# Kernel tuning notes

Measured on AMD Instinct MI355X. Metric: run time of the kernel, lower is better.

The kernel has to match this reference:

```python
import jax, jax.numpy as jnp
import numpy as np


def setup_inputs() -> dict:
    key = jax.random.key(0)
    ks = jax.random.split(key, 5)
    B, T, C, H, E = 8, 2048, 1024, 2048, 8
    n_layer = 12
    x = jax.random.normal(ks[0], (B, T, C), dtype=jnp.float32)
    w_router = jax.random.normal(ks[1], (C, E), dtype=jnp.float32) * 0.02
    w_c_fc = jax.random.normal(ks[2], (E, C, H), dtype=jnp.float32) * 0.02
    w_gate = jax.random.normal(ks[3], (E, C, H), dtype=jnp.float32) * 0.02
    w_c_proj = jax.random.normal(ks[4], (E, H, C), dtype=jnp.float32) * (0.02 * (2 * n_layer) ** -0.5)
    return {
        "x": x, "w_router": w_router, "w_c_fc": w_c_fc,
        "w_gate": w_gate, "w_c_proj": w_c_proj,
        "top_k": 2, "n_experts": E, "expert_capacity": 640,
    }


def reference(x, w_router, w_c_fc, w_gate, w_c_proj, top_k, n_experts, expert_capacity):
    B, T, C = x.shape
    # ---- router ----
    gate_logits = jnp.einsum('btc,ce->bte', x, w_router)
    gate_probs = jax.nn.softmax(gate_logits, axis=-1)  # (B,T,E)

    # ---- per-batch top-k dispatch (cumsum slot assignment + scatter) ----
    def dispatch(xb, pb):
        # xb: (T,C), pb: (T,E)
        topk_p, topk_i = jax.lax.top_k(pb, top_k)              # (T,k)
        ei = jnp.swapaxes(topk_i, 0, 1).ravel()                # (k*T,) k-major
        oh = jax.nn.one_hot(ei, n_experts, dtype=jnp.int32)    # (k*T,E)
        pos = jnp.cumsum(oh, axis=0) * oh - 1                  # slot within expert
        pos = jnp.swapaxes(pos.reshape(top_k, T, n_experts), 0, 1).max(axis=2)  # (T,k)
        ei = jnp.swapaxes(ei.reshape(top_k, T), 0, 1)          # (T,k)
        buf = jnp.zeros((n_experts, expert_capacity, C), dtype=xb.dtype)
        xr = jnp.repeat(xb, top_k, axis=0)                     # (T*k,C) token-major
        buf = buf.at[ei.ravel(), pos.ravel()].set(xr)          # overflow slots dropped
        return topk_p, pos, ei, buf

    topk_p, pos, ei, buf = jax.vmap(dispatch)(x, gate_probs)   # buf: (B,E,cap,C)

    # ---- batched expert SwiGLU GEMMs ----
    ein = jnp.swapaxes(buf, 0, 1).reshape(n_experts, B * expert_capacity, C)
    h = jnp.einsum('eti,eih->eth', ein, w_c_fc)
    g = jax.nn.silu(jnp.einsum('eti,eih->eth', ein, w_gate))
    o = jnp.einsum('eth,eho->eto', g * h, w_c_proj)
    eo = jnp.swapaxes(o.reshape(n_experts, B, expert_capacity, C), 0, 1)  # (B,E,cap,C)

    # ---- weighted combine gather ----
    def combine(eo_b, i_b, p_b, pr_b):
        sel = eo_b[i_b, p_b]                                   # (T,k,C)
        return jnp.sum(pr_b[..., None] * sel, axis=1)          # (T,C)

    y = jax.vmap(combine)(eo, ei, pos, topk_p)                 # (B,T,C)
    return y
```

## Files before the change

### kernel.cpp

```cpp
#include <hip/hip_runtime.h>
#include <stdint.h>

#define B_   8
#define T_   2048
#define C_   1024
#define H_   2048
#define E_   8
#define CAP_ 640
#define RPE_ (B_*CAP_)
#define BT_  (B_*T_)

typedef __attribute__((ext_vector_type(8))) short bf16x8;
typedef __attribute__((ext_vector_type(4))) float f32x4;

static __device__ __forceinline__ unsigned short f2bf(float f){
  union { float f; uint32_t u; } a; a.f = f;
  uint32_t u = a.u;
  uint32_t r = (u + 0x7FFFu + ((u >> 16) & 1u)) >> 16;
  return (unsigned short)r;
}

#define GLD16(gp, lp) __builtin_amdgcn_global_load_lds( \
    (__attribute__((address_space(1))) void*)(gp), \
    (__attribute__((address_space(3))) void*)(lp), 16, 0, 0)

#define VMW(N) asm volatile("s_waitcnt vmcnt(" #N ")" ::: "memory")
#define FENCE  asm volatile("" ::: "memory")
#define BARS   do { FENCE; __builtin_amdgcn_s_barrier(); __builtin_amdgcn_sched_barrier(0); } while(0)
#define BARE   do { __builtin_amdgcn_sched_barrier(0); FENCE; __builtin_amdgcn_s_barrier(); FENCE; } while(0)

#define LDA(H) do { \
  _Pragma("unroll") for (int ks_=0; ks_<2; ++ks_) \
  _Pragma("unroll") for (int f_=0; f_<4; ++f_) \
    pa[ks_][f_] = *(const bf16x8*)(bufc + (H)*16384u + aRow + (unsigned)f_*2048u + cc[ks_]); \
} while(0)
#define LDB(PB, H) do { \
  _Pragma("unroll") for (int ks_=0; ks_<2; ++ks_) \
  _Pragma("unroll") for (int n_=0; n_<2; ++n_) \
    PB[ks_][n_] = *(const bf16x8*)(bufc + 32768u + (H)*16384u + bRow + (unsigned)n_*2048u + cc[ks_]); \
} while(0)
#define MM16(Q, PB) do { \
  __builtin_amdgcn_s_setprio(1); \
  _Pragma("unroll") for (int ks_=0; ks_<2; ++ks_) \
  _Pragma("unroll") for (int f_=0; f_<4; ++f_) \
  _Pragma("unroll") for (int n_=0; n_<2; ++n_) \
    acc[Q][f_][n_] = __builtin_amdgcn_mfma_f32_16x16x32_bf16(pa[ks_][f_], PB[ks_][n_], acc[Q][f_][n_], 0,0,0); \
  __builtin_amdgcn_s_setprio(0); \
} while(0)

#define STG_A(H, T1) do { \
  unsigned kb_ = (unsigned)(T1)*128u; \
  unsigned db_ = ((unsigned)(T1)&1u)*65536u + (H)*16384u; \
  GLD16(pA##H##0 + kb_, lds + db_ + d0); \
  GLD16(pA##H##1 + kb_, lds + db_ + 8192u + d0); \
} while(0)
#define STG_B(H, T1) do { \
  unsigned kb_ = (unsigned)(T1)*128u; \
  unsigned db_ = ((unsigned)(T1)&1u)*65536u + 32768u + (H)*16384u; \
  GLD16(pB##H##0 + kb_, lds + db_ + d0); \
  GLD16(pB##H##1 + kb_, lds + db_ + 8192u + d0); \
} while(0)

#define STG2_A(H, T2, BI) do { \
  unsigned kb_ = (unsigned)(T2)*128u; \
  unsigned db_ = (unsigned)(BI)*49152u + (H)*16384u; \
  GLD16(pA##H##0 + kb_, lds + db_ + d0); \
  GLD16(pA##H##1 + kb_, lds + db_ + 8192u + d0); \
} while(0)
#define STG2_B(T2, BI) do { \
  unsigned kb_ = (unsigned)(T2)*128u; \
  unsigned db_ = (unsigned)(BI)*49152u + 32768u; \
  GLD16(pB00 + kb_, lds + db_ + d0); \
  GLD16(pB01 + kb_, lds + db_ + 8192u + d0); \
} while(0)

__global__ __launch_bounds__(256) void router_kernel(
    const float* __restrict__ x, const float* __restrict__ wr,
    unsigned short* __restrict__ xbf, float* __restrict__ probs2, int* __restrict__ idx2)
{
  int bt = blockIdx.x;
  int tid = threadIdx.x;
  const float4 v = ((const float4*)(x + (size_t)bt*C_))[tid];
  ushort4 u;
  u.x = f2bf(v.x); u.y = f2bf(v.y); u.z = f2bf(v.z); u.w = f2bf(v.w);
  ((ushort4*)(xbf + (size_t)bt*C_))[tid] = u;

  double p[8];
  #pragma unroll
  for (int e=0;e<8;e++) p[e]=0.0;
  const float xv[4] = {v.x, v.y, v.z, v.w};
  #pragma unroll
  for (int j=0;j<4;j++){
    int c = tid*4+j;
    const float* wrow = wr + c*8;
    #pragma unroll
    for (int e=0;e<8;e++) p[e] += (double)xv[j] * (double)wrow[e];
  }
  __shared__ double red[8][256];
  #pragma unroll
  for (int e=0;e<8;e++) red[e][tid] = p[e];
  __syncthreads();
  for (int s=128; s>0; s>>=1){
    if (tid < s){
      #pragma unroll
      for (int e=0;e<8;e++) red[e][tid] += red[e][tid+s];
    }
    __syncthreads();
  }
  if (tid==0){
    double lg[8];
    #pragma unroll
    for (int e=0;e<8;e++) lg[e]=red[e][0];
    double mx = lg[0];
    #pragma unroll
    for (int e=1;e<8;e++) if (lg[e]>mx) mx=lg[e];
    double s=0.0, ex[8];
    #pragma unroll
    for (int e=0;e<8;e++){ ex[e]=exp(lg[e]-mx); s+=ex[e]; }
    int i1=0; double b1=ex[0];
    #pragma unroll
    for (int e=1;e<8;e++) if (ex[e]>b1){ b1=ex[e]; i1=e; }
    int i2=-1; double b2=-1.0;
    #pragma unroll
    for (int e=0;e<8;e++) if (e!=i1 && ex[e]>b2){ b2=ex[e]; i2=e; }
    probs2[bt*2+0] = (float)(b1/s);
    probs2[bt*2+1] = (float)(b2/s);
    idx2[bt*2+0] = i1;
    idx2[bt*2+1] = i2;
  }
}

__global__ __launch_bounds__(256) void transp_fcg_kernel(
    const float* __restrict__ fc, const float* __restrict__ gate,
    unsigned short* __restrict__ dst)
{
  __shared__ float t[32][33];
  int e = blockIdx.z;
  int n0 = blockIdx.x*32, k0 = blockIdx.y*32;
  int tx = threadIdx.x & 31, ty = threadIdx.x >> 5;
  #pragma unroll
  for (int sel=0; sel<2; ++sel){
    const float* s = (sel ? gate : fc) + ((size_t)e*C_ + k0)*H_ + n0;
    #pragma unroll
    for (int i=0;i<32;i+=8) t[ty+i][tx] = s[(size_t)(ty+i)*H_ + tx];
    __syncthreads();
    #pragma unroll
    for (int i=0;i<32;i+=8){
      int jj = ty+i;
      int drow = n0*2 + ((jj & 16) << 1) + sel*16 + (jj & 15);
      dst[((size_t)e*4096 + drow)*1024 + k0 + tx] = f2bf(t[tx][jj]);
    }
    __syncthreads();
  }
}

__global__ __launch_bounds__(256) void transp_kernel(
    const float* __restrict__ src, unsigned short* __restrict__ dst, int K, int N)
{
  __shared__ float t[32][33];
  int e = blockIdx.z;
  int n0 = blockIdx.x*32, k0 = blockIdx.y*32;
  int tx = threadIdx.x & 31, ty = threadIdx.x >> 5;
  const float* s = src + ((size_t)e*K + k0)*N + n0;
  #pragma unroll
  for (int i=0;i<32;i+=8) t[ty+i][tx] = s[(size_t)(ty+i)*N + tx];
  __syncthreads();
  unsigned short* d = dst + ((size_t)e*N + n0)*K + k0;
  #pragma unroll
  for (int i=0;i<32;i+=8) d[(size_t)(ty+i)*K + tx] = f2bf(t[tx][ty+i]);
}

__global__ void scan_kernel(const int* __restrict__ idx2, int* __restrict__ pos, int* __restrict__ cnt)
{
  int b = blockIdx.x, lane = threadIdx.x;
  unsigned long long below = (lane == 0) ? 0ull : (~0ull >> (64 - lane));
  int base = 0;
  for (int k=0;k<2;k++){
    for (int c0=0;c0<T_;c0+=64){
      int t = c0 + lane;
      int e = idx2[((b*T_ + t)<<1) + k];
      unsigned long long mym = 0; int addv = 0;
      #pragma unroll
      for (int ee=0; ee<8; ++ee){
        unsigned long long m = __ballot(e == ee);
        if (ee == e) mym = m;
        if (lane == ee) addv = __popcll(m);
      }
      int mybase = __shfl(base, e, 64);
      pos[((b*T_+t)<<1)+k] = mybase + __popcll(mym & below);
      base += addv;
    }
  }
  if (lane < 8) cnt[b*8 + lane] = (base < CAP_) ? base : CAP_;
}

__global__ void offsets_kernel(const int* __restrict__ cnt, int* __restrict__ off, int* __restrict__ Me)
{
  int e = threadIdx.x;
  if (e < 8){
    int s = 0;
    for (int b=0;b<8;b++){ off[e*8+b] = s; s += cnt[b*8+e]; }
    Me[e] = s;
  }
}

__global__ void fill_kernel(const int* __restrict__ idx2, const int* __restrict__ pos,
                            const int* __restrict__ off, const float* __restrict__ probs2,
                            int* __restrict__ token_src, float* __restrict__ row_prob)
{
  int a = blockIdx.x*256 + threadIdx.x;
  if (a >= BT_*2) return;
  int bt = a >> 1, k = a & 1;
  int b = bt >> 11;
  int e = idx2[bt*2+k];
  int p = pos[bt*2+k];
  if (p < CAP_){
    int r = e*RPE_ + off[e*8+b] + p;
    token_src[r] = bt;
    row_prob[r] = probs2[bt*2+k];
  }
}

__global__ __launch_bounds__(512, 2) void gemm1_kernel(
    const unsigned short* __restrict__ xbf,
    const unsigned short* __restrict__ wifcg,
    const int* __restrict__ token_src,
    const int* __restrict__ Me,
    unsigned short* __restrict__ act,
    int e0)
{
  const int lin = blockIdx.x;
  const int ez = lin / 320;
  const int r_ = lin % 320;
  const int xcd = r_ & 7, slot = r_ >> 3;
  const int nt = xcd + ((slot / 20) << 3);
  const int mt = slot % 20;
  const int e = e0 + ez;
  const int M = Me[e];
  if (mt*256 >= M) return;

  __shared__ __align__(16) unsigned char lds[131072];

  const int tid = threadIdx.x;
  const int w = tid >> 6, l = tid & 63;
  const int wm = w >> 2, wn = w & 3;
  const int l15 = l & 15, g0 = l >> 4;
  const unsigned d0 = (unsigned)tid * 16u;

  const int srow0 = tid >> 3, c0 = tid & 7;
  const unsigned scb = (unsigned)((c0 ^ (srow0 & 7)) * 16);
  const unsigned char* gA = (const unsigned char*)xbf;
  const unsigned char* gB = (const unsigned char*)wifcg;
  const int abase = e*RPE_ + mt*256;
  const unsigned char* pA00 = gA + (size_t)token_src[abase +       srow0]*2048u + scb;
  const unsigned char* pA01 = gA + (size_t)token_src[abase +  64 + srow0]*2048u + scb;
  const unsigned char* pA10 = gA + (size_t)token_src[abase + 128 + srow0]*2048u + scb;
  const unsigned char* pA11 = gA + (size_t)token_src[abase + 192 + srow0]*2048u + scb;
  const size_t bbase = (size_t)(ez*4096 + nt*256 + srow0);
  const unsigned char* pB00 = gB + (bbase +   0)*2048u + scb;
  const unsigned char* pB01 = gB + (bbase +  64)*2048u + scb;
  const unsigned char* pB10 = gB + (bbase + 128)*2048u + scb;
  const unsigned char* pB11 = gB + (bbase + 192)*2048u + scb;

  const unsigned aRow = (unsigned)((wm*64 + l15) * 128);
  const unsigned bRow = (unsigned)((wn*32 + l15) * 128);
  unsigned cc[2];
  cc[0] = (unsigned)(((0*4 + g0) ^ (l15 & 7)) * 16);
  cc[1] = (unsigned)(((1*4 + g0) ^ (l15 & 7)) * 16);

  f32x4 acc[4][4][2];
  #pragma unroll
  for (int p=0;p<4;++p)
    #pragma unroll
    for (int f=0;f<4;++f)
      #pragma unroll
      for (int n=0;n<2;++n) acc[p][f][n] = (f32x4){0.f,0.f,0.f,0.f};

  bf16x8 pa[2][4], pb0[2][2], pb1[2][2];

  STG_A(0,0); STG_B(0,0); STG_B(1,0); STG_A(1,0);
  VMW(4);
  FENCE; __builtin_amdgcn_s_barrier(); FENCE;

  const int NT = 16;
  for (int t = 0; t < NT-1; ++t){
    const unsigned char* bufc = lds + (unsigned)(t&1)*65536u;
    LDA(0); LDB(pb0,0); STG_A(0,t+1); VMW(4); BARS; MM16(0,pb0); BARE;
    LDB(pb1,1);         STG_B(0,t+1); VMW(4); BARS; MM16(1,pb1); BARE;
    LDA(1);             STG_B(1,t+1);         BARS; MM16(2,pb0); BARE;
                        STG_A(1,t+1); VMW(4); BARS; MM16(3,pb1); BARE;
  }
  {
    const unsigned char* bufc = lds + (unsigned)((NT-1)&1)*65536u;
    LDA(0); LDB(pb0,0); VMW(2); BARS; MM16(0,pb0); BARE;
    LDB(pb1,1);         VMW(0); BARS; MM16(1,pb1); BARE;
    LDA(1);                     BARS; MM16(2,pb0); BARE;
                                BARS; MM16(3,pb1); BARE;
  }

  const int r4 = (l >> 4) * 4;
  #pragma unroll
  for (int p=0;p<4;++p){
    const int ah = p>>1, bh = p&1;
    #pragma unroll
    for (int f=0;f<4;++f){
      const int grow = mt*256 + ah*128 + wm*64 + f*16 + r4;
      const int hcol = nt*128 + bh*64 + wn*16 + l15;
      #pragma unroll
      for (int r=0;r<4;++r){
        float h = acc[p][f][0][r];
        float gv = acc[p][f][1][r];
        float a = (gv / (1.f + __expf(-gv))) * h;
        act[((size_t)ez*RPE_ + grow + r)*(size_t)H_ + hcol] = f2bf(a);
      }
    }
  }
}

__global__ __launch_bounds__(512, 2) void gemm2_kernel(
    const unsigned short* __restrict__ act,
    const unsigned short* __restrict__ wprojT,
    const int* __restrict__ token_src,
    const float* __restrict__ row_prob,
    const int* __restrict__ Me,
    float* __restrict__ y,
    int e0)
{
  const int lin = blockIdx.x;
  const int ez = lin / 192;
  const int r_ = lin % 192;
  const int xcd = r_ & 7, slot = r_ >> 3;
  const int mt = xcd + ((slot >> 3) << 3);
  const int nt = slot & 7;
  if (mt >= 20) return;
  const int e = e0 + ez;
  const int M = Me[e];
  if (mt*256 >= M) return;

  __shared__ __align__(16) unsigned char lds[147456];

  const int tid = threadIdx.x;
  const int w = tid >> 6, l = tid & 63;
  const int wm = w >> 2, wn = w & 3;
  const int l15 = l & 15, g0 = l >> 4;
  const unsigned d0 = (unsigned)tid * 16u;

  const int srow0 = tid >> 3, c0 = tid & 7;
  const unsigned scb = (unsigned)((c0 ^ (srow0 & 7)) * 16);
  const unsigned char* gA = (const unsigned char*)act;
  const unsigned char* gB = (const unsigned char*)wprojT;
  const size_t abase = (size_t)(ez*RPE_ + mt*256 + srow0);
  const unsigned char* pA00 = gA + (abase +   0)*4096u + scb;
  const unsigned char* pA01 = gA + (abase +  64)*4096u + scb;
  const unsigned char* pA10 = gA + (abase + 128)*4096u + scb;
  const unsigned char* pA11 = gA + (abase + 192)*4096u + scb;
  const size_t bbase = (size_t)(ez*C_ + nt*128 + srow0);
  const unsigned char* pB00 = gB + (bbase +   0)*4096u + scb;
  const unsigned char* pB01 = gB + (bbase +  64)*4096u + scb;

  const unsigned aRow = (unsigned)((wm*64 + l15) * 128);
  const unsigned bRow = (unsigned)((wn*32 + l15) * 128);
  unsigned cc[2];
  cc[0] = (unsigned)(((0*4 + g0) ^ (l15 & 7)) * 16);
  cc[1] = (unsigned)(((1*4 + g0) ^ (l15 & 7)) * 16);

  f32x4 acc[2][4][2];
  #pragma unroll
  for (int p=0;p<2;++p)
    #pragma unroll
    for (int f=0;f<4;++f)
      #pragma unroll
      for (int n=0;n<2;++n) acc[p][f][n] = (f32x4){0.f,0.f,0.f,0.f};

  bf16x8 pa[2][4], pb[2][2];

  STG2_A(0,0,0); STG2_B(0,0); STG2_A(1,0,0);
  STG2_A(0,1,1); STG2_B(1,1); STG2_A(1,1,1);
  VMW(8);
  FENCE; __builtin_amdgcn_s_barrier(); FENCE;

  const int NT = 32;
  for (int t = 0; t < NT-2; ++t){
    const unsigned char* bufc = lds + (unsigned)(t%3)*49152u;
    const int bi2 = (t+2)%3;
    LDA(0); LDB(pb,0); STG2_A(0,t+2,bi2); STG2_B(t+2,bi2); VMW(10); BARS; MM16(0,pb); BARE;
    LDA(1);            STG2_A(1,t+2,bi2);                  VMW(8);  BARS; MM16(1,pb); BARE;
  }
  {
    const unsigned char* bufc = lds + (unsigned)((NT-2)%3)*49152u;
    LDA(0); LDB(pb,0); VMW(6); BARS; MM16(0,pb); BARE;
    LDA(1);            VMW(2); BARS; MM16(1,pb); BARE;
  }
  {
    const unsigned char* bufc = lds + (unsigned)((NT-1)%3)*49152u;
    LDA(0); LDB(pb,0); VMW(0); BARS; MM16(0,pb); BARE;
    LDA(1);                    BARS; MM16(1,pb); BARE;
  }

  const int r4 = (l >> 4) * 4;
  #pragma unroll
  for (int p=0;p<2;++p){
    #pragma unroll
    for (int f=0;f<4;++f){
      #pragma unroll
      for (int r=0;r<4;++r){
        const int rloc = mt*256 + p*128 + wm*64 + f*16 + r4 + r;
        if (rloc < M){
          const int bt = token_src[e*RPE_ + rloc];
          const float pp = row_prob[e*RPE_ + rloc];
          float* yrow = y + (size_t)bt*C_;
          const int colb = nt*128 + wn*32 + l15;
          atomicAdd(yrow + colb,      pp * acc[p][f][0][r]);
          atomicAdd(yrow + colb + 16, pp * acc[p][f][1][r]);
        }
      }
    }
  }
}

extern "C" void kernel_launch(void* const* d_in, const int* in_sizes, int n_in,
                              void* d_out, int out_size, void* d_ws, size_t ws_size,
                              hipStream_t stream)
{
  const float* x   = (const float*)d_in[0];
  const float* wr  = (const float*)d_in[1];
  const float* wfc = (const float*)d_in[2];
  const float* wg  = (const float*)d_in[3];
  const float* wpj = (const float*)d_in[4];
  float* y = (float*)d_out;

  unsigned char* ws = (unsigned char*)d_ws;
  const size_t szXBF  = (size_t)BT_*C_*2;
  const size_t szFCGc = (size_t)2*4096*1024*2;
  const size_t szWPc  = (size_t)2*C_*H_*2;
  const size_t szFCGa = (size_t)E_*4096*1024*2;
  const size_t szWPa  = (size_t)E_*C_*H_*2;
  const size_t szMISC = 3*131072 + 2*(size_t)E_*RPE_*4 + 1024;

  const size_t need_small = szXBF + szFCGc + szWPc + (size_t)2*RPE_*H_*2 + szMISC;
  const size_t need_big2  = szXBF + szFCGa + szWPa  + (size_t)2*RPE_*H_*2 + szMISC;
  const size_t need_big4  = szXBF + szFCGa + szWPa  + (size_t)4*RPE_*H_*2 + szMISC;
  if (ws_size < need_small) return;
  const bool big4 = (ws_size >= need_big4);
  const bool big  = big4 || (ws_size >= need_big2);
  const int  ne   = big4 ? 4 : 2;

  const size_t szFCG = big ? szFCGa : szFCGc;
  const size_t szWP  = big ? szWPa  : szWPc;
  const size_t szACT = (size_t)ne*RPE_*H_*2;

  size_t oXBF = 0;
  size_t oFCG = oXBF + szXBF;
  size_t oWP  = oFCG + szFCG;
  size_t oACT = oWP  + szWP;
  size_t oM   = oACT + szACT;

  unsigned short* xbf    = (unsigned short*)(ws + oXBF);
  unsigned short* wifcg  = (unsigned short*)(ws + oFCG);
  unsigned short* wprojT = (unsigned short*)(ws + oWP);
  unsigned short* actc   = (unsigned short*)(ws + oACT);

  float* probs2    = (float*)(ws + oM);
  int*   idx2      = (int*)(ws + oM + 1*131072);
  int*   pos       = (int*)(ws + oM + 2*131072);
  int*   token_src = (int*)(ws + oM + 3*131072);
  float* row_prob  = (float*)(ws + oM + 3*131072 + (size_t)E_*RPE_*4);
  int*   cnt       = (int*)(ws + oM + 3*131072 + 2*(size_t)E_*RPE_*4);
  int*   off       = cnt + 64;
  int*   Me        = off + 64;

  hipMemsetAsync(y, 0, (size_t)out_size*4, stream);
  hipMemsetAsync(token_src, 0, (size_t)E_*RPE_*4, stream);

  router_kernel<<<BT_, 256, 0, stream>>>(x, wr, xbf, probs2, idx2);
  scan_kernel<<<B_, 64, 0, stream>>>(idx2, pos, cnt);
  offsets_kernel<<<1, 64, 0, stream>>>(cnt, off, Me);
  fill_kernel<<<(BT_*2+255)/256, 256, 0, stream>>>(idx2, pos, off, probs2, token_src, row_prob);

  if (big){
    transp_fcg_kernel<<<dim3(H_/32, C_/32, E_), 256, 0, stream>>>(wfc, wg, wifcg);
    transp_kernel<<<dim3(C_/32, H_/32, E_), 256, 0, stream>>>(wpj, wprojT, H_, C_);
  }

  for (int e0 = 0; e0 < E_; e0 += ne){
    unsigned short* wfcg_c = wifcg;
    unsigned short* wpj_c  = wprojT;
    if (big){
      wfcg_c = wifcg  + (size_t)e0*4096*1024;
      wpj_c  = wprojT + (size_t)e0*C_*H_;
    } else {
      transp_fcg_kernel<<<dim3(H_/32, C_/32, ne), 256, 0, stream>>>(
          wfc + (size_t)e0*C_*H_, wg + (size_t)e0*C_*H_, wifcg);
      transp_kernel<<<dim3(C_/32, H_/32, ne), 256, 0, stream>>>(
          wpj + (size_t)e0*H_*C_, wprojT, H_, C_);
    }
    gemm1_kernel<<<dim3(320*ne), 512, 0, stream>>>(
        xbf, wfcg_c, token_src, Me, actc, e0);
    gemm2_kernel<<<dim3(192*ne), 512, 0, stream>>>(
        actc, wpj_c, token_src, row_prob, Me, y, e0);
  }
}
```

Measured before the change: 768.9 us.

## Switch gemm2 to double-buffered LDS pipeline and plain 3D grid

Changes gemm2's pipeline from a three-stage LDS ring to a two-stage double buffer, shrinking shared memory from 144KB to 96KB and prefetching one tile ahead instead of two. It also drops the XCD-aware swizzled 1D block mapping in favour of a straightforward (nt, mt, expert) 3D grid. The smaller LDS footprint may allow better occupancy, but the change gives up prefetch depth and the L2 locality the XCD swizzle provided.

```diff
diff --git a/kernel.cpp b/kernel.cpp
--- a/kernel.cpp
+++ b/kernel.cpp
@@ -61,17 +61,22 @@
   GLD16(pB##H##1 + kb_, lds + db_ + 8192u + d0); \
 } while(0)
 
-#define STG2_A(H, T2, BI) do { \
-  unsigned kb_ = (unsigned)(T2)*128u; \
-  unsigned db_ = (unsigned)(BI)*49152u + (H)*16384u; \
+#define SG2A(H, T1) do { \
+  unsigned kb_ = (unsigned)(T1)*128u; \
+  unsigned db_ = ((unsigned)(T1)&1u)*49152u + (H)*16384u; \
   GLD16(pA##H##0 + kb_, lds + db_ + d0); \
   GLD16(pA##H##1 + kb_, lds + db_ + 8192u + d0); \
 } while(0)
-#define STG2_B(T2, BI) do { \
-  unsigned kb_ = (unsigned)(T2)*128u; \
-  unsigned db_ = (unsigned)(BI)*49152u + 32768u; \
+#define SG2B(T1) do { \
+  unsigned kb_ = (unsigned)(T1)*128u; \
+  unsigned db_ = ((unsigned)(T1)&1u)*49152u + 32768u; \
   GLD16(pB00 + kb_, lds + db_ + d0); \
   GLD16(pB01 + kb_, lds + db_ + 8192u + d0); \
+} while(0)
+#define LDB2 do { \
+  _Pragma("unroll") for (int ks_=0; ks_<2; ++ks_) \
+  _Pragma("unroll") for (int n_=0; n_<2; ++n_) \
+    pb[ks_][n_] = *(const bf16x8*)(bufc + 32768u + bRow + (unsigned)n_*2048u + cc[ks_]); \
 } while(0)
 
 __global__ __launch_bounds__(256) void router_kernel(
@@ -326,18 +331,11 @@
     float* __restrict__ y,
     int e0)
 {
-  const int lin = blockIdx.x;
-  const int ez = lin / 192;
-  const int r_ = lin % 192;
-  const int xcd = r_ & 7, slot = r_ >> 3;
-  const int mt = xcd + ((slot >> 3) << 3);
-  const int nt = slot & 7;
-  if (mt >= 20) return;
-  const int e = e0 + ez;
+  const int ez = blockIdx.z, e = e0 + ez, mt = blockIdx.y, nt = blockIdx.x;
   const int M = Me[e];
   if (mt*256 >= M) return;
 
-  __shared__ __align__(16) unsigned char lds[147456];
+  __shared__ __align__(16) unsigned char lds[98304];
 
   const int tid = threadIdx.x;
   const int w = tid >> 6, l = tid & 63;
@@ -374,27 +372,20 @@
 
   bf16x8 pa[2][4], pb[2][2];
 
-  STG2_A(0,0,0); STG2_B(0,0); STG2_A(1,0,0);
-  STG2_A(0,1,1); STG2_B(1,1); STG2_A(1,1,1);
-  VMW(8);
+  SG2A(0,0); SG2B(0); SG2A(1,0);
+  VMW(2);
   FENCE; __builtin_amdgcn_s_barrier(); FENCE;
 
   const int NT = 32;
-  for (int t = 0; t < NT-2; ++t){
-    const unsigned char* bufc = lds + (unsigned)(t%3)*49152u;
-    const int bi2 = (t+2)%3;
-    LDA(0); LDB(pb,0); STG2_A(0,t+2,bi2); STG2_B(t+2,bi2); VMW(10); BARS; MM16(0,pb); BARE;
-    LDA(1);            STG2_A(1,t+2,bi2);                  VMW(8);  BARS; MM16(1,pb); BARE;
+  for (int t = 0; t < NT-1; ++t){
+    const unsigned char* bufc = lds + (unsigned)(t&1)*49152u;
+    LDA(0); LDB2; SG2A(0,t+1); SG2B(t+1); VMW(4); BARS; MM16(0,pb); BARE;
+    LDA(1);       SG2A(1,t+1);           VMW(2); BARS; MM16(1,pb); BARE;
   }
   {
-    const unsigned char* bufc = lds + (unsigned)((NT-2)%3)*49152u;
-    LDA(0); LDB(pb,0); VMW(6); BARS; MM16(0,pb); BARE;
-    LDA(1);            VMW(2); BARS; MM16(1,pb); BARE;
-  }
-  {
-    const unsigned char* bufc = lds + (unsigned)((NT-1)%3)*49152u;
-    LDA(0); LDB(pb,0); VMW(0); BARS; MM16(0,pb); BARE;
-    LDA(1);                    BARS; MM16(1,pb); BARE;
+    const unsigned char* bufc = lds + (unsigned)((NT-1)&1)*49152u;
+    LDA(0); LDB2; VMW(0); BARS; MM16(0,pb); BARE;
+    LDA(1);               BARS; MM16(1,pb); BARE;
   }
 
   const int r4 = (l >> 4) * 4;
@@ -496,7 +487,7 @@
     }
     gemm1_kernel<<<dim3(320*ne), 512, 0, stream>>>(
         xbf, wfcg_c, token_src, Me, actc, e0);
-    gemm2_kernel<<<dim3(192*ne), 512, 0, stream>>>(
+    gemm2_kernel<<<dim3(8, 20, ne), 512, 0, stream>>>(
         actc, wpj_c, token_src, row_prob, Me, y, e0);
   }
 }
```

After: 800.0 us. 1.04x slower.
